# Kernel optimization log

Hardware: AMD Instinct MI355X
Metric: run time of the kernel (lower is better)

## Reference

```python
import jax, jax.numpy as jnp
import numpy as np

D_MODEL = 512
N_HEAD = 8
D_K = 64
D_V = 64
NUM_FEATURES = 266  # round(d_k * ln(d_k)) for d_k=64
KERNEL_EPS = 1e-4
NORM_STAB = 1e-6
LN_EPS = 1e-6


def _orthogonal_random_features():
    # blocks of transposed Q factors of Gaussian matrices, scaled by sqrt(d_k)
    rng = np.random.default_rng(0)
    blocks, rows = [], NUM_FEATURES
    while rows > 0:
        g = rng.standard_normal((D_K, D_K)).astype(np.float32)
        qm, _ = np.linalg.qr(g)
        blocks.append(qm.T[: min(rows, D_K)])
        rows -= D_K
    rf = np.concatenate(blocks, axis=0) * np.sqrt(D_K)
    return jnp.asarray(rf, dtype=jnp.float32)  # [m, d_k]


def _xavier(key, fan_in, fan_out):
    a = np.sqrt(6.0 / (fan_in + fan_out))
    return jax.random.uniform(key, (fan_in, fan_out), jnp.float32, -a, a)


def setup_inputs() -> dict:
    key = jax.random.key(0)
    ks = jax.random.split(key, 9)
    B, N = 1, 2048
    return {
        "q": jax.random.normal(ks[0], (B, N, D_MODEL), jnp.float32),
        "k": jax.random.normal(ks[1], (B, N, D_MODEL), jnp.float32),
        "v": jax.random.normal(ks[2], (B, N, D_MODEL), jnp.float32),
        "Wq": _xavier(ks[3], D_MODEL, N_HEAD * D_K),
        "Wk": _xavier(ks[4], D_MODEL, N_HEAD * D_K),
        "Wv": _xavier(ks[5], D_MODEL, N_HEAD * D_V),
        "W_fc": _xavier(ks[6], N_HEAD * D_V, D_MODEL),
        "b_fc": jnp.zeros((D_MODEL,), jnp.float32),
        "gamma": jnp.ones((D_MODEL,), jnp.float32),
        "beta": jnp.zeros((D_MODEL,), jnp.float32),
        "rf": _orthogonal_random_features(),
    }


def reference(q, k, v, Wq, Wk, Wv, W_fc, b_fc, gamma, beta, rf):
    B, N, _ = q.shape
    residual = q
    # pre-layernorm on queries only (normalize_before=True)
    mu = jnp.mean(q, axis=-1, keepdims=True)
    var = jnp.mean((q - mu) ** 2, axis=-1, keepdims=True)
    qn = (q - mu) * jax.lax.rsqrt(var + LN_EPS) * gamma + beta

    def heads(x, W, d):
        return (x @ W).reshape(B, N, N_HEAD, d).transpose(0, 2, 1, 3)

    qh = heads(qn, Wq, D_K)   # [b,h,n,dk]
    kh = heads(k, Wk, D_K)
    vh = heads(v, Wv, D_V)    # [b,h,n,dv]

    scale = D_MODEL ** (-0.25)
    qh = qh * scale
    kh = kh * scale

    proj_q = jnp.einsum('bhnd,md->bhnm', qh, rf)  # [b,h,n,m]
    proj_k = jnp.einsum('bhnd,md->bhnm', kh, rf)
    h_q = -0.5 * jnp.sum(qh ** 2, axis=-1, keepdims=True)  # [b,h,n,1]
    h_k = -0.5 * jnp.sum(kh ** 2, axis=-1, keepdims=True)

    # per-query stabilizer is h_q itself (last dim of h_q has size 1)
    q_kernel = jnp.exp(h_q + (proj_q - h_q))
    k_stab = jnp.max(h_k)  # global max stabilizer for keys
    k_kernel = jnp.exp(h_k + (proj_k - k_stab))

    c = NUM_FEATURES ** (-0.5)
    q_prime = c * (q_kernel + KERNEL_EPS)
    k_prime = c * (k_kernel + KERNEL_EPS)

    # causal linear attention via prefix sums
    D_inv = 1.0 / jnp.einsum('bhnm,bhnm->bhn', q_prime, jnp.cumsum(k_prime, axis=2))
    context = jnp.cumsum(jnp.einsum('bhnm,bhne->bhnme', k_prime, vh), axis=2)  # [b,h,n,m,dv]
    out = jnp.einsum('bhnme,bhnm,bhn->bhne', context, q_prime, D_inv)

    # output normalization with stabilizer
    d = jnp.einsum('bhnm,bhm->bhn', q_prime, jnp.sum(k_prime, axis=2))[..., None]
    d = d + 2.0 * NORM_STAB * (jnp.abs(d) <= NORM_STAB).astype(d.dtype)
    out = out / d

    out = out.transpose(0, 2, 1, 3).reshape(B, N, N_HEAD * D_V)
    return out @ W_fc + b_fc + residual
```

## Files before the change

kernel.cpp:

```cpp
#include <hip/hip_runtime.h>
#include <hip/hip_bf16.h>
#include <math.h>

#define DMODEL 512
#define NSEQ 2048
#define NHEAD 8
#define DK 64
#define DV 64
#define MFEAT 266
#define MPAD 288
#define NT 32
#define LN_EPS 1e-6f
#define KERNEL_EPS 1e-4f
#define NORM_STAB 1e-6f
#define SCALE 0.21022410381342863f

typedef __attribute__((ext_vector_type(8))) short short8;
typedef __attribute__((ext_vector_type(4))) short sv4;
typedef __attribute__((ext_vector_type(4))) float f32x4;

__device__ inline short f2bf(float f) {
    return (short)__bfloat16_as_ushort(__float2bfloat16(f));
}
__device__ inline float bf2f(short s) {
    unsigned u = ((unsigned)(unsigned short)s) << 16;
    return __builtin_bit_cast(float, u);
}

__global__ __launch_bounds__(256) void prep_kernel(const float* __restrict__ Wq,
                                                   const float* __restrict__ Wk,
                                                   const float* __restrict__ Wv,
                                                   const float* __restrict__ Wfc,
                                                   const float* __restrict__ rf,
                                                   short* __restrict__ Wqt,
                                                   short* __restrict__ Wkt,
                                                   short* __restrict__ Wvt,
                                                   short* __restrict__ Wfct,
                                                   short* __restrict__ rfb) {
    int wsel = blockIdx.z;
    int tid = threadIdx.x;
    if (wsel == 4) {
        if (blockIdx.x != 0) return;
        int r0 = blockIdx.y * 36;
        for (int lp = 0; lp < 9; ++lp) {
            int c = tid + lp * 256;
            int r = r0 + c / 64, d = c % 64;
            float v = (r < MFEAT) ? rf[(size_t)r * DK + d] : 0.f;
            rfb[(size_t)r * DK + d] = f2bf(v);
        }
        return;
    }
    __shared__ short T[64][65];
    int k0 = blockIdx.x * 64, n0 = blockIdx.y * 64;
    const float* W = (wsel == 0) ? Wq : (wsel == 1) ? Wk : (wsel == 2) ? Wv : Wfc;
    short* Wt = (wsel == 0) ? Wqt : (wsel == 1) ? Wkt : (wsel == 2) ? Wvt : Wfct;
    float scale = (wsel <= 1) ? SCALE : 1.f;
    for (int lp = 0; lp < 4; ++lp) {
        int c = tid + lp * 256;
        int kk = c >> 4, q4 = (c & 15) * 4;
        f32x4 v = *(const f32x4*)&W[(size_t)(k0 + kk) * DMODEL + n0 + q4];
        for (int j = 0; j < 4; ++j) T[q4 + j][kk] = f2bf(v[j] * scale);
    }
    __syncthreads();
    for (int lp = 0; lp < 2; ++lp) {
        int c = tid + lp * 256;
        int nn = c >> 3, c8 = c & 7;
        short8 v = *(const short8*)&T[nn][c8 * 8];
        *(short8*)&Wt[(size_t)(n0 + nn) * DMODEL + k0 + c8 * 8] = v;
    }
}

__global__ __launch_bounds__(256) void qkvfeat_kernel(const float* __restrict__ qx,
                                                      const float* __restrict__ kx,
                                                      const float* __restrict__ vx,
                                                      const short* __restrict__ Wqt,
                                                      const short* __restrict__ Wkt,
                                                      const short* __restrict__ Wvt,
                                                      const float* __restrict__ gamma,
                                                      const float* __restrict__ beta,
                                                      const short* __restrict__ rfb,
                                                      short* __restrict__ vh,
                                                      short* __restrict__ qp,
                                                      short* __restrict__ kp) {
    __shared__ __align__(16) char smem[38656];
    auto AsB = (short(*)[40])smem;
    auto BsB = (short(*)[40])(smem + 10240);
    auto Xs = (short(*)[72])smem;
    short* kpl = (short*)smem;
    float* hks = (float*)(smem + 38400);

    int z = blockIdx.z;
    const float* A = (z == 0) ? qx : (z == 1) ? kx : vx;
    const short* Bt = (z == 0) ? Wqt : (z == 1) ? Wkt : Wvt;
    int nt = blockIdx.x, h = blockIdx.y;
    int bm = nt * 64, bn = h * 64, n0 = nt * 64;
    int tid = threadIdx.x;
    int wid = tid >> 6, lane = tid & 63;
    f32x4 acc[4] = {f32x4{0,0,0,0}, f32x4{0,0,0,0}, f32x4{0,0,0,0}, f32x4{0,0,0,0}};
    int ar = tid >> 2, akq = tid & 3;
    float lnm = 0.f, lnr = 0.f;
    if (z == 0) {
        const float* xr = qx + (size_t)(bm + ar) * DMODEL + akq * 128;
        float s = 0.f, ss = 0.f;
#pragma unroll 4
        for (int i = 0; i < 128; i += 4) {
            f32x4 vv = *(const f32x4*)(xr + i);
            s += vv[0] + vv[1] + vv[2] + vv[3];
            ss += vv[0]*vv[0] + vv[1]*vv[1] + vv[2]*vv[2] + vv[3]*vv[3];
        }
        s += __shfl_xor(s, 1); s += __shfl_xor(s, 2);
        ss += __shfl_xor(ss, 1); ss += __shfl_xor(ss, 2);
        float m = s / (float)DMODEL;
        float var = ss / (float)DMODEL - m * m;
        lnm = m;
        lnr = rsqrtf(var + LN_EPS);
    }
    auto loadA = [&](int k0) -> short8 {
        const float* src = A + (size_t)(bm + ar) * DMODEL + k0 + akq * 8;
        f32x4 v0 = *(const f32x4*)src;
        f32x4 v1 = *(const f32x4*)(src + 4);
        short8 sv;
        if (z == 0) {
            f32x4 g0 = *(const f32x4*)&gamma[k0 + akq * 8];
            f32x4 g1 = *(const f32x4*)&gamma[k0 + akq * 8 + 4];
            f32x4 bb0 = *(const f32x4*)&beta[k0 + akq * 8];
            f32x4 bb1 = *(const f32x4*)&beta[k0 + akq * 8 + 4];
            for (int j = 0; j < 4; ++j) {
                sv[j] = f2bf((v0[j] - lnm) * lnr * g0[j] + bb0[j]);
                sv[4 + j] = f2bf((v1[j] - lnm) * lnr * g1[j] + bb1[j]);
            }
        } else {
            for (int j = 0; j < 4; ++j) { sv[j] = f2bf(v0[j]); sv[4 + j] = f2bf(v1[j]); }
        }
        return sv;
    };
    auto loadB = [&](int k0) -> short8 {
        return *(const short8*)&Bt[(size_t)(bn + ar) * DMODEL + k0 + akq * 8];
    };
    short8 aR0 = loadA(0), bR0 = loadB(0);
    short8 aR1 = loadA(32), bR1 = loadB(32);
    int buf = 0;
#pragma unroll 2
    for (int k0 = 0; k0 < DMODEL; k0 += 32) {
        int slot = (k0 >> 5) & 1;
        if (slot == 0) {
            *(short8*)&AsB[buf * 64 + ar][akq * 8] = aR0;
            *(short8*)&BsB[buf * 64 + ar][akq * 8] = bR0;
        } else {
            *(short8*)&AsB[buf * 64 + ar][akq * 8] = aR1;
            *(short8*)&BsB[buf * 64 + ar][akq * 8] = bR1;
        }
        __syncthreads();
        if (k0 + 64 < DMODEL) {
            if (slot == 0) { aR0 = loadA(k0 + 64); bR0 = loadB(k0 + 64); }
            else           { aR1 = loadA(k0 + 64); bR1 = loadB(k0 + 64); }
        }
        int row = buf * 64 + wid * 16 + (lane & 15);
        int koff = (lane >> 4) * 8;
        short8 a = *(const short8*)&AsB[row][koff];
        for (int nf = 0; nf < 4; ++nf) {
            int col = buf * 64 + nf * 16 + (lane & 15);
            short8 b = *(const short8*)&BsB[col][koff];
            acc[nf] = __builtin_amdgcn_mfma_f32_16x16x32_bf16(a, b, acc[nf], 0, 0, 0);
        }
        buf ^= 1;
    }
    __syncthreads();
    if (z == 2) {
        for (int nf = 0; nf < 4; ++nf) {
            int col = bn + nf * 16 + (lane & 15);
            for (int j = 0; j < 4; ++j) {
                int row = bm + wid * 16 + (lane >> 4) * 4 + j;
                vh[(size_t)row * DMODEL + col] = f2bf(acc[nf][j]);
            }
        }
        return;
    }
    for (int nf = 0; nf < 4; ++nf) {
        int col = nf * 16 + (lane & 15);
        for (int j = 0; j < 4; ++j) {
            int row = wid * 16 + (lane >> 4) * 4 + j;
            Xs[row][col] = f2bf(acc[nf][j]);
        }
    }
    if (z == 1) {
        for (int j = 0; j < 4; ++j) {
            float ss = 0.f;
            for (int nf = 0; nf < 4; ++nf) ss += acc[nf][j] * acc[nf][j];
            for (int o = 1; o < 16; o <<= 1) ss += __shfl_xor(ss, o);
            if ((lane & 15) == 0) hks[wid * 16 + (lane >> 4) * 4 + j] = -0.5f * ss;
        }
    }
    __syncthreads();

    int w = wid, l = lane;
    int fr = l & 15, fq = (l >> 4) * 8;
    short8 xb0 = *(const short8*)&Xs[w * 16 + fr][fq];
    short8 xb1 = *(const short8*)&Xs[w * 16 + fr][32 + fq];
    int n_loc = w * 16 + fr;
    float hval = (z == 1) ? hks[n_loc] : 0.f;
    __syncthreads();

    short (*kpl2)[300] = (short(*)[300])kpl;
    const float cnorm = 0.06131393394849658f;
#pragma unroll
    for (int tr = 0; tr < 18; ++tr) {
        int row = tr * 16 + fr;
        short8 a0 = *(const short8*)&rfb[(size_t)row * DK + fq];
        short8 a1 = *(const short8*)&rfb[(size_t)row * DK + 32 + fq];
        f32x4 facc = {0.f, 0.f, 0.f, 0.f};
        facc = __builtin_amdgcn_mfma_f32_16x16x32_bf16(a0, xb0, facc, 0, 0, 0);
        facc = __builtin_amdgcn_mfma_f32_16x16x32_bf16(a1, xb1, facc, 0, 0, 0);
        sv4 o;
        for (int j = 0; j < 4; ++j) {
            int m = tr * 16 + (l >> 4) * 4 + j;
            float val = (m < MFEAT) ? cnorm * (__expf(facc[j] + hval) + KERNEL_EPS) : 0.f;
            o[j] = f2bf(val);
        }
        *(sv4*)&kpl2[n_loc][tr * 16 + (l >> 4) * 4] = o;
    }
    __syncthreads();
    short* outp = (z == 0) ? qp : kp;
    for (int lp = 0; lp < 9; ++lp) {
        int c = tid + lp * 256;
        int nn = c / 36, c8 = c % 36;
        short8 v = *(const short8*)&kpl2[nn][c8 * 8];
        *(short8*)&outp[((size_t)h * NSEQ + n0 + nn) * MPAD + c8 * 8] = v;
    }
}

__global__ __launch_bounds__(256) void chunksum_kernel(const short* __restrict__ kp,
                                                       const short* __restrict__ vh,
                                                       short* __restrict__ KVc,
                                                       float* __restrict__ Ks) {
    int t = blockIdx.x, h = blockIdx.y;
    __shared__ short kpT[288 * 72];
    __shared__ short Vt[64][72];
    int tid = threadIdx.x;
    int w = tid >> 6, l = tid & 63;
    int fr = l & 15, fq8 = (l >> 4) * 8;
    const short* kpb = kp + ((size_t)h * NSEQ + (size_t)t * 64) * MPAD;

    for (int lp = 0; lp < 9; ++lp) {
        int c = tid + lp * 256;
        int i = c / 36, c8 = c % 36;
        short8 v = *(const short8*)&kpb[(size_t)i * MPAD + c8 * 8];
        int i8 = i >> 3, i7 = i & 7;
        for (int jj = 0; jj < 8; ++jj) {
            int m = c8 * 8 + jj;
            int ig = i8 ^ ((m >> 3) & 7);
            kpT[m * 72 + ig * 8 + i7] = v[jj];
        }
    }
    for (int lp = 0; lp < 2; ++lp) {
        int c = tid + lp * 256;
        int i = c & 63, d8 = (c >> 6) * 8;
        short8 v = *(const short8*)&vh[(size_t)(t * 64 + i) * DMODEL + h * DV + d8];
        for (int jj = 0; jj < 8; ++jj) Vt[d8 + jj][i] = v[jj];
    }
    __syncthreads();

    f32x4 acc[5][4];
#pragma unroll
    for (int tt = 0; tt < 5; ++tt)
        for (int nf = 0; nf < 4; ++nf) acc[tt][nf] = f32x4{0, 0, 0, 0};
#pragma unroll
    for (int tt = 0; tt < 5; ++tt) {
        int tr = w + tt * 4;
        if (tr < 18) {
            int row = tr * 16 + fr;
            int swz = (row >> 3) & 7;
            short8 a0 = *(const short8*)&kpT[row * 72 + (((fq8 >> 3)) ^ swz) * 8];
            short8 a1 = *(const short8*)&kpT[row * 72 + ((4 + (fq8 >> 3)) ^ swz) * 8];
            for (int nf = 0; nf < 4; ++nf) {
                short8 b0 = *(const short8*)&Vt[nf * 16 + fr][fq8];
                short8 b1 = *(const short8*)&Vt[nf * 16 + fr][32 + fq8];
                acc[tt][nf] = __builtin_amdgcn_mfma_f32_16x16x32_bf16(a0, b0, acc[tt][nf], 0, 0, 0);
                acc[tt][nf] = __builtin_amdgcn_mfma_f32_16x16x32_bf16(a1, b1, acc[tt][nf], 0, 0, 0);
            }
        }
    }
    for (int m = tid; m < MPAD; m += 256) {
        int swz = (m >> 3) & 7;
        float s = 0.f;
        for (int i8 = 0; i8 < 8; ++i8) {
            int ig = i8 ^ swz;
            for (int j = 0; j < 8; ++j) s += bf2f(kpT[m * 72 + ig * 8 + j]);
        }
        Ks[((size_t)h * NT + t) * MPAD + m] = s;
    }
    __syncthreads();
    short* kvT = kpT;
#pragma unroll
    for (int tt = 0; tt < 5; ++tt) {
        int tr = w + tt * 4;
        if (tr < 18) {
            for (int nf = 0; nf < 4; ++nf) {
                int dv = nf * 16 + fr;
                for (int j = 0; j < 4; ++j) {
                    int m = tr * 16 + (l >> 4) * 4 + j;
                    kvT[dv * 296 + m] = f2bf(acc[tt][nf][j]);
                }
            }
        }
    }
    __syncthreads();
    for (int lp = 0; lp < 9; ++lp) {
        int c = tid + lp * 256;
        int dv = c / 36, c8 = c % 36;
        short8 v = *(const short8*)&kvT[dv * 296 + c8 * 8];
        *(short8*)&KVc[(((size_t)h * NT + t) * DV + dv) * MPAD + c8 * 8] = v;
    }
}

__global__ __launch_bounds__(256) void scan_kernel(const short* __restrict__ KVc,
                                                   short* __restrict__ KVbT,
                                                   float* __restrict__ Ks,
                                                   float* __restrict__ Ktot) {
    int idx = blockIdx.x * 256 + threadIdx.x;
    const int NKV = NHEAD * DV * MPAD;
    if (idx < NKV) {
        int h = idx / (DV * MPAD);
        int rem = idx % (DV * MPAD);
        size_t base = (size_t)h * NT * DV * MPAD + rem;
        short vals[NT];
#pragma unroll
        for (int t = 0; t < NT; ++t) vals[t] = KVc[base + (size_t)t * DV * MPAD];
        float run = 0.f;
#pragma unroll
        for (int t = 0; t < NT; ++t) {
            KVbT[base + (size_t)t * DV * MPAD] = f2bf(run);
            run += bf2f(vals[t]);
        }
    } else {
        int j = idx - NKV;
        if (j < NHEAD * MPAD) {
            int h = j / MPAD, m = j % MPAD;
            size_t base = (size_t)h * NT * MPAD + m;
            float vals[NT];
#pragma unroll
            for (int t = 0; t < NT; ++t) vals[t] = Ks[base + (size_t)t * MPAD];
            float run = 0.f;
#pragma unroll
            for (int t = 0; t < NT; ++t) {
                Ks[base + (size_t)t * MPAD] = run;
                run += vals[t];
            }
            Ktot[(size_t)h * MPAD + m] = run;
        }
    }
}

__global__ __launch_bounds__(256) void phasec_kernel(const short* __restrict__ qp,
                                                     const short* __restrict__ kp,
                                                     const short* __restrict__ vh,
                                                     const short* __restrict__ KVbT,
                                                     const float* __restrict__ Ks,
                                                     const float* __restrict__ Ktot,
                                                     short* __restrict__ attn) {
    int t = blockIdx.x, h = blockIdx.y;
    __shared__ short Buf[64][296];
    __shared__ short Vt[64][72];
    __shared__ short Am[64][72];
    __shared__ float Ksp[MPAD], Ktp[MPAD];
    __shared__ float fscale_s[64];
    int tid = threadIdx.x;
    int w = tid >> 6, l = tid & 63;
    int fr = l & 15, fq = (l >> 4) * 8;
    const short* qpb = qp + ((size_t)h * NSEQ + (size_t)t * 64) * MPAD;
    const short* kpb = kp + ((size_t)h * NSEQ + (size_t)t * 64) * MPAD;
    const short* stb = KVbT + ((size_t)h * NT + t) * DV * MPAD;

    short8 qf[9];
#pragma unroll
    for (int ks = 0; ks < 9; ++ks)
        qf[ks] = *(const short8*)&qpb[(size_t)(w * 16 + fr) * MPAD + ks * 32 + fq];

    int srow = tid >> 2, sc4 = tid & 3;
#pragma unroll
    for (int lp = 0; lp < 9; ++lp) {
        int c = sc4 + lp * 4;
        *(short8*)&Buf[srow][c * 8] = *(const short8*)&kpb[(size_t)srow * MPAD + c * 8];
    }
    for (int lp = 0; lp < 2; ++lp) {
        int c = tid + lp * 256;
        int i = c & 63, d8 = (c >> 6) * 8;
        short8 v = *(const short8*)&vh[(size_t)(t * 64 + i) * DMODEL + h * DV + d8];
        for (int jj = 0; jj < 8; ++jj) Vt[d8 + jj][i] = v[jj];
    }
    for (int idx = tid; idx < MPAD; idx += 256) {
        Ksp[idx] = Ks[((size_t)h * NT + t) * MPAD + idx];
        Ktp[idx] = Ktot[(size_t)h * MPAD + idx];
    }
    short8 stg[9];
#pragma unroll
    for (int lp = 0; lp < 9; ++lp) {
        int c = sc4 + lp * 4;
        stg[lp] = *(const short8*)&stb[(size_t)srow * MPAD + c * 8];
    }
    __syncthreads();

    f32x4 accA[4] = {f32x4{0,0,0,0}, f32x4{0,0,0,0}, f32x4{0,0,0,0}, f32x4{0,0,0,0}};
    f32x4 accO[4] = {f32x4{0,0,0,0}, f32x4{0,0,0,0}, f32x4{0,0,0,0}, f32x4{0,0,0,0}};
#pragma unroll 3
    for (int ks = 0; ks < 9; ++ks) {
        int ko = ks * 32 + fq;
        for (int nf = 0; nf < 4; ++nf) {
            short8 bk = *(const short8*)&Buf[nf * 16 + fr][ko];
            accA[nf] = __builtin_amdgcn_mfma_f32_16x16x32_bf16(qf[ks], bk, accA[nf], 0, 0, 0);
        }
    }
    __syncthreads();
#pragma unroll
    for (int lp = 0; lp < 9; ++lp) {
        int c = sc4 + lp * 4;
        *(short8*)&Buf[srow][c * 8] = stg[lp];
    }
    for (int nf = 0; nf < 4; ++nf) {
        int col = nf * 16 + fr;
        for (int j = 0; j < 4; ++j) {
            int row = w * 16 + (l >> 4) * 4 + j;
            Am[row][col] = (col <= row) ? f2bf(accA[nf][j]) : (short)0;
        }
    }
    __syncthreads();
#pragma unroll 3
    for (int ks = 0; ks < 9; ++ks) {
        int ko = ks * 32 + fq;
        for (int nf = 0; nf < 4; ++nf) {
            short8 bs = *(const short8*)&Buf[nf * 16 + fr][ko];
            accO[nf] = __builtin_amdgcn_mfma_f32_16x16x32_bf16(qf[ks], bs, accO[nf], 0, 0, 0);
        }
    }
#pragma unroll
    for (int ks = 0; ks < 2; ++ks) {
        int ko = ks * 32 + fq;
        short8 a = *(const short8*)&Am[w * 16 + fr][ko];
        for (int nf = 0; nf < 4; ++nf) {
            short8 b = *(const short8*)&Vt[nf * 16 + fr][ko];
            accO[nf] = __builtin_amdgcn_mfma_f32_16x16x32_bf16(a, b, accO[nf], 0, 0, 0);
        }
    }
    int di = tid >> 2, dp = tid & 3;
    float dc = 0.f, df = 0.f;
    {
        const short* amrow = &Am[di][dp * 16];
        short8 s0 = *(const short8*)amrow;
        short8 s1 = *(const short8*)(amrow + 8);
        for (int j2 = 0; j2 < 8; ++j2) dc += bf2f(s0[j2]) + bf2f(s1[j2]);
    }
#pragma unroll
    for (int c8 = 0; c8 < 9; ++c8) {
        int m = dp * 72 + c8 * 8;
        short8 qv = *(const short8*)&qpb[(size_t)di * MPAD + m];
        for (int j2 = 0; j2 < 8; ++j2) {
            float qq = bf2f(qv[j2]);
            dc += qq * Ksp[m + j2];
            df += qq * Ktp[m + j2];
        }
    }
    dc += __shfl_xor(dc, 1); dc += __shfl_xor(dc, 2);
    df += __shfl_xor(df, 1); df += __shfl_xor(df, 2);
    if (dp == 0) {
        float dst = df;
        if (fabsf(dst) <= NORM_STAB) dst += 2.f * NORM_STAB;
        fscale_s[di] = (1.f / dc) / dst;
    }
    __syncthreads();
    for (int nf = 0; nf < 4; ++nf) {
        int col = nf * 16 + fr;
        for (int j = 0; j < 4; ++j) {
            int row = w * 16 + (l >> 4) * 4 + j;
            attn[((size_t)t * 64 + row) * DMODEL + h * DV + col] =
                f2bf(accO[nf][j] * fscale_s[row]);
        }
    }
}

__global__ __launch_bounds__(256) void fgemm_kernel(const short* __restrict__ A,
                                                    const short* __restrict__ Bt,
                                                    float* __restrict__ C,
                                                    const float* __restrict__ bias,
                                                    const float* __restrict__ residual) {
    __shared__ short AsB[128][40];
    __shared__ short BsB[128][40];
    int bm = blockIdx.y * 64, bn = blockIdx.x * 64;
    int tid = threadIdx.x;
    int wid = tid >> 6, lane = tid & 63;
    f32x4 acc[4] = {f32x4{0,0,0,0}, f32x4{0,0,0,0}, f32x4{0,0,0,0}, f32x4{0,0,0,0}};
    int ar = tid >> 2, akq = tid & 3;
    auto ldA = [&](int k0) { return *(const short8*)&A[(size_t)(bm + ar) * DMODEL + k0 + akq * 8]; };
    auto ldB = [&](int k0) { return *(const short8*)&Bt[(size_t)(bn + ar) * DMODEL + k0 + akq * 8]; };
    short8 aR0 = ldA(0), bR0 = ldB(0);
    short8 aR1 = ldA(32), bR1 = ldB(32);
    int buf = 0;
#pragma unroll 2
    for (int k0 = 0; k0 < DMODEL; k0 += 32) {
        int slot = (k0 >> 5) & 1;
        if (slot == 0) {
            *(short8*)&AsB[buf * 64 + ar][akq * 8] = aR0;
            *(short8*)&BsB[buf * 64 + ar][akq * 8] = bR0;
        } else {
            *(short8*)&AsB[buf * 64 + ar][akq * 8] = aR1;
            *(short8*)&BsB[buf * 64 + ar][akq * 8] = bR1;
        }
        __syncthreads();
        if (k0 + 64 < DMODEL) {
            if (slot == 0) { aR0 = ldA(k0 + 64); bR0 = ldB(k0 + 64); }
            else           { aR1 = ldA(k0 + 64); bR1 = ldB(k0 + 64); }
        }
        int row = buf * 64 + wid * 16 + (lane & 15);
        int koff = (lane >> 4) * 8;
        short8 a = *(const short8*)&AsB[row][koff];
        for (int nf = 0; nf < 4; ++nf) {
            int col = buf * 64 + nf * 16 + (lane & 15);
            short8 b = *(const short8*)&BsB[col][koff];
            acc[nf] = __builtin_amdgcn_mfma_f32_16x16x32_bf16(a, b, acc[nf], 0, 0, 0);
        }
        buf ^= 1;
    }
    for (int nf = 0; nf < 4; ++nf) {
        int col = bn + nf * 16 + (lane & 15);
        for (int j = 0; j < 4; ++j) {
            int row = bm + wid * 16 + (lane >> 4) * 4 + j;
            C[(size_t)row * DMODEL + col] =
                acc[nf][j] + bias[col] + residual[(size_t)row * DMODEL + col];
        }
    }
}

extern "C" void kernel_launch(void* const* d_in, const int* in_sizes, int n_in,
                              void* d_out, int out_size, void* d_ws, size_t ws_size,
                              hipStream_t stream) {
    const float* q = (const float*)d_in[0];
    const float* k = (const float*)d_in[1];
    const float* v = (const float*)d_in[2];
    const float* Wq = (const float*)d_in[3];
    const float* Wk = (const float*)d_in[4];
    const float* Wv = (const float*)d_in[5];
    const float* Wfc = (const float*)d_in[6];
    const float* bfc = (const float*)d_in[7];
    const float* gamma = (const float*)d_in[8];
    const float* beta = (const float*)d_in[9];
    const float* rf = (const float*)d_in[10];
    float* out = (float*)d_out;

    float* ws = (float*)d_ws;
    short* attn = (short*)ws;
    short* vhb = attn + (size_t)NSEQ * DMODEL;
    short* qp = vhb + (size_t)NSEQ * DMODEL;
    short* kp = qp + (size_t)NHEAD * NSEQ * MPAD;
    short* KVc = kp + (size_t)NHEAD * NSEQ * MPAD;
    short* KVbT = KVc + (size_t)NHEAD * NT * DV * MPAD;
    float* Ks = (float*)(KVbT + (size_t)NHEAD * NT * DV * MPAD);
    float* Ktot = Ks + (size_t)NHEAD * NT * MPAD;
    short* Wqt = (short*)(Ktot + (size_t)NHEAD * MPAD);
    short* Wkt = Wqt + (size_t)DMODEL * DMODEL;
    short* Wvt = Wkt + (size_t)DMODEL * DMODEL;
    short* Wfct = Wvt + (size_t)DMODEL * DMODEL;
    short* rfb = Wfct + (size_t)DMODEL * DMODEL;

    dim3 gp(8, 8, 5);
    prep_kernel<<<gp, 256, 0, stream>>>(Wq, Wk, Wv, Wfc, rf, Wqt, Wkt, Wvt, Wfct, rfb);
    dim3 gq(NT, NHEAD, 3);
    qkvfeat_kernel<<<gq, 256, 0, stream>>>(q, k, v, Wqt, Wkt, Wvt, gamma, beta, rfb,
                                           vhb, qp, kp);
    dim3 ga(NT, NHEAD);
    chunksum_kernel<<<ga, 256, 0, stream>>>(kp, vhb, KVc, Ks);
    int scan_threads = NHEAD * DV * MPAD + NHEAD * MPAD;
    scan_kernel<<<(scan_threads + 255) / 256, 256, 0, stream>>>(KVc, KVbT, Ks, Ktot);
    dim3 gc(NT, NHEAD);
    phasec_kernel<<<gc, 256, 0, stream>>>(qp, kp, vhb, KVbT, Ks, Ktot, attn);
    dim3 g(DMODEL / 64, NSEQ / 64);
    fgemm_kernel<<<g, 256, 0, stream>>>(attn, Wfct, out, bfc, q);
}
```

Baseline: 70.49 us.

## Halve qkvfeat row tile to 32 rows and split waves over columns and features

The fused QKV projection and feature kernel now handles 32 sequence rows per block instead of 64, which doubles the grid to 64x8x3 blocks. The four waves are rearranged into a 2x2 grid over rows and output columns, and the feature loop is split between wave pairs. The squared norm for the key stabiliser is reduced across waves through shared memory. The aim is more blocks, better occupancy and less shared memory per block on a small problem. The cost is more redundant weight and rf loads per output row and a shallower register prefetch (one stage instead of two).

```diff
diff --git a/kernel.cpp b/kernel.cpp
--- a/kernel.cpp
+++ b/kernel.cpp
@@ -82,130 +82,116 @@
                                                       short* __restrict__ vh,
                                                       short* __restrict__ qp,
                                                       short* __restrict__ kp) {
-    __shared__ __align__(16) char smem[38656];
+    __shared__ __align__(16) char smem[19712];
     auto AsB = (short(*)[40])smem;
-    auto BsB = (short(*)[40])(smem + 10240);
+    auto BsB = (short(*)[40])(smem + 5120);
     auto Xs = (short(*)[72])smem;
     short* kpl = (short*)smem;
-    float* hks = (float*)(smem + 38400);
+    float* hks = (float*)(smem + 19200);
+    float* hpart = (float*)(smem + 19328);
 
     int z = blockIdx.z;
     const float* A = (z == 0) ? qx : (z == 1) ? kx : vx;
     const short* Bt = (z == 0) ? Wqt : (z == 1) ? Wkt : Wvt;
     int nt = blockIdx.x, h = blockIdx.y;
-    int bm = nt * 64, bn = h * 64, n0 = nt * 64;
+    int bm = nt * 32, bn = h * 64;
     int tid = threadIdx.x;
     int wid = tid >> 6, lane = tid & 63;
-    f32x4 acc[4] = {f32x4{0,0,0,0}, f32x4{0,0,0,0}, f32x4{0,0,0,0}, f32x4{0,0,0,0}};
-    int ar = tid >> 2, akq = tid & 3;
+    int fr = lane & 15, fq = (lane >> 4) * 8;
+    int rt = wid & 1, cfb = (wid >> 1) * 2;
+    f32x4 acc[2] = {f32x4{0,0,0,0}, f32x4{0,0,0,0}};
+    int arow = tid >> 3, ak = tid & 7;
+    int nrow = tid >> 2, bk = (tid & 3) * 8;
     float lnm = 0.f, lnr = 0.f;
     if (z == 0) {
-        const float* xr = qx + (size_t)(bm + ar) * DMODEL + akq * 128;
+        const float* xr = qx + (size_t)(bm + arow) * DMODEL + ak * 64;
         float s = 0.f, ss = 0.f;
 #pragma unroll 4
-        for (int i = 0; i < 128; i += 4) {
+        for (int i = 0; i < 64; i += 4) {
             f32x4 vv = *(const f32x4*)(xr + i);
             s += vv[0] + vv[1] + vv[2] + vv[3];
             ss += vv[0]*vv[0] + vv[1]*vv[1] + vv[2]*vv[2] + vv[3]*vv[3];
         }
-        s += __shfl_xor(s, 1); s += __shfl_xor(s, 2);
-        ss += __shfl_xor(ss, 1); ss += __shfl_xor(ss, 2);
+        s += __shfl_xor(s, 1); s += __shfl_xor(s, 2); s += __shfl_xor(s, 4);
+        ss += __shfl_xor(ss, 1); ss += __shfl_xor(ss, 2); ss += __shfl_xor(ss, 4);
         float m = s / (float)DMODEL;
         float var = ss / (float)DMODEL - m * m;
         lnm = m;
         lnr = rsqrtf(var + LN_EPS);
     }
-    auto loadA = [&](int k0) -> short8 {
-        const float* src = A + (size_t)(bm + ar) * DMODEL + k0 + akq * 8;
-        f32x4 v0 = *(const f32x4*)src;
-        f32x4 v1 = *(const f32x4*)(src + 4);
-        short8 sv;
+    auto loadA = [&](int k0) -> sv4 {
+        f32x4 v0 = *(const f32x4*)&A[(size_t)(bm + arow) * DMODEL + k0 + ak * 4];
+        sv4 sv;
         if (z == 0) {
-            f32x4 g0 = *(const f32x4*)&gamma[k0 + akq * 8];
-            f32x4 g1 = *(const f32x4*)&gamma[k0 + akq * 8 + 4];
-            f32x4 bb0 = *(const f32x4*)&beta[k0 + akq * 8];
-            f32x4 bb1 = *(const f32x4*)&beta[k0 + akq * 8 + 4];
-            for (int j = 0; j < 4; ++j) {
-                sv[j] = f2bf((v0[j] - lnm) * lnr * g0[j] + bb0[j]);
-                sv[4 + j] = f2bf((v1[j] - lnm) * lnr * g1[j] + bb1[j]);
-            }
+            f32x4 g0 = *(const f32x4*)&gamma[k0 + ak * 4];
+            f32x4 b0 = *(const f32x4*)&beta[k0 + ak * 4];
+            for (int j = 0; j < 4; ++j)
+                sv[j] = f2bf((v0[j] - lnm) * lnr * g0[j] + b0[j]);
         } else {
-            for (int j = 0; j < 4; ++j) { sv[j] = f2bf(v0[j]); sv[4 + j] = f2bf(v1[j]); }
+            for (int j = 0; j < 4; ++j) sv[j] = f2bf(v0[j]);
         }
         return sv;
     };
     auto loadB = [&](int k0) -> short8 {
-        return *(const short8*)&Bt[(size_t)(bn + ar) * DMODEL + k0 + akq * 8];
+        return *(const short8*)&Bt[(size_t)(bn + nrow) * DMODEL + k0 + bk];
     };
-    short8 aR0 = loadA(0), bR0 = loadB(0);
-    short8 aR1 = loadA(32), bR1 = loadB(32);
+    sv4 aReg = loadA(0);
+    short8 bReg = loadB(0);
     int buf = 0;
 #pragma unroll 2
     for (int k0 = 0; k0 < DMODEL; k0 += 32) {
-        int slot = (k0 >> 5) & 1;
-        if (slot == 0) {
-            *(short8*)&AsB[buf * 64 + ar][akq * 8] = aR0;
-            *(short8*)&BsB[buf * 64 + ar][akq * 8] = bR0;
-        } else {
-            *(short8*)&AsB[buf * 64 + ar][akq * 8] = aR1;
-            *(short8*)&BsB[buf * 64 + ar][akq * 8] = bR1;
-        }
+        *(sv4*)&AsB[buf * 32 + arow][ak * 4] = aReg;
+        *(short8*)&BsB[buf * 64 + nrow][bk] = bReg;
         __syncthreads();
-        if (k0 + 64 < DMODEL) {
-            if (slot == 0) { aR0 = loadA(k0 + 64); bR0 = loadB(k0 + 64); }
-            else           { aR1 = loadA(k0 + 64); bR1 = loadB(k0 + 64); }
-        }
-        int row = buf * 64 + wid * 16 + (lane & 15);
-        int koff = (lane >> 4) * 8;
-        short8 a = *(const short8*)&AsB[row][koff];
-        for (int nf = 0; nf < 4; ++nf) {
-            int col = buf * 64 + nf * 16 + (lane & 15);
-            short8 b = *(const short8*)&BsB[col][koff];
+        if (k0 + 32 < DMODEL) { aReg = loadA(k0 + 32); bReg = loadB(k0 + 32); }
+        short8 a = *(const short8*)&AsB[buf * 32 + rt * 16 + fr][fq];
+        for (int nf = 0; nf < 2; ++nf) {
+            short8 b = *(const short8*)&BsB[buf * 64 + (cfb + nf) * 16 + fr][fq];
             acc[nf] = __builtin_amdgcn_mfma_f32_16x16x32_bf16(a, b, acc[nf], 0, 0, 0);
         }
         buf ^= 1;
     }
     __syncthreads();
     if (z == 2) {
-        for (int nf = 0; nf < 4; ++nf) {
-            int col = bn + nf * 16 + (lane & 15);
+        for (int nf = 0; nf < 2; ++nf) {
+            int col = bn + (cfb + nf) * 16 + fr;
             for (int j = 0; j < 4; ++j) {
-                int row = bm + wid * 16 + (lane >> 4) * 4 + j;
+                int row = bm + rt * 16 + (lane >> 4) * 4 + j;
                 vh[(size_t)row * DMODEL + col] = f2bf(acc[nf][j]);
             }
         }
         return;
     }
-    for (int nf = 0; nf < 4; ++nf) {
-        int col = nf * 16 + (lane & 15);
-        for (int j = 0; j < 4; ++j) {
-            int row = wid * 16 + (lane >> 4) * 4 + j;
-            Xs[row][col] = f2bf(acc[nf][j]);
-        }
+    for (int nf = 0; nf < 2; ++nf) {
+        int col = (cfb + nf) * 16 + fr;
+        for (int j = 0; j < 4; ++j)
+            Xs[rt * 16 + (lane >> 4) * 4 + j][col] = f2bf(acc[nf][j]);
     }
     if (z == 1) {
         for (int j = 0; j < 4; ++j) {
-            float ss = 0.f;
-            for (int nf = 0; nf < 4; ++nf) ss += acc[nf][j] * acc[nf][j];
+            float ss = acc[0][j] * acc[0][j] + acc[1][j] * acc[1][j];
             for (int o = 1; o < 16; o <<= 1) ss += __shfl_xor(ss, o);
-            if ((lane & 15) == 0) hks[wid * 16 + (lane >> 4) * 4 + j] = -0.5f * ss;
-        }
-    }
-    __syncthreads();
-
-    int w = wid, l = lane;
-    int fr = l & 15, fq = (l >> 4) * 8;
-    short8 xb0 = *(const short8*)&Xs[w * 16 + fr][fq];
-    short8 xb1 = *(const short8*)&Xs[w * 16 + fr][32 + fq];
-    int n_loc = w * 16 + fr;
+            if (fr == 0) hpart[(rt * 16 + (lane >> 4) * 4 + j) * 2 + (wid >> 1)] = ss;
+        }
+    }
+    __syncthreads();
+    if (z == 1 && tid < 32)
+        hks[tid] = -0.5f * (hpart[tid * 2] + hpart[tid * 2 + 1]);
+    __syncthreads();
+
+    int nb = wid & 1, mpar = wid >> 1;
+    int n_loc = nb * 16 + fr;
+    short8 xb0 = *(const short8*)&Xs[n_loc][fq];
+    short8 xb1 = *(const short8*)&Xs[n_loc][32 + fq];
     float hval = (z == 1) ? hks[n_loc] : 0.f;
     __syncthreads();
 
     short (*kpl2)[300] = (short(*)[300])kpl;
     const float cnorm = 0.06131393394849658f;
 #pragma unroll
-    for (int tr = 0; tr < 18; ++tr) {
-        int row = tr * 16 + fr;
+    for (int t = 0; t < 9; ++t) {
+        int mt = mpar + 2 * t;
+        int row = mt * 16 + fr;
         short8 a0 = *(const short8*)&rfb[(size_t)row * DK + fq];
         short8 a1 = *(const short8*)&rfb[(size_t)row * DK + 32 + fq];
         f32x4 facc = {0.f, 0.f, 0.f, 0.f};
@@ -213,19 +199,21 @@
         facc = __builtin_amdgcn_mfma_f32_16x16x32_bf16(a1, xb1, facc, 0, 0, 0);
         sv4 o;
         for (int j = 0; j < 4; ++j) {
-            int m = tr * 16 + (l >> 4) * 4 + j;
+            int m = mt * 16 + (lane >> 4) * 4 + j;
             float val = (m < MFEAT) ? cnorm * (__expf(facc[j] + hval) + KERNEL_EPS) : 0.f;
             o[j] = f2bf(val);
         }
-        *(sv4*)&kpl2[n_loc][tr * 16 + (l >> 4) * 4] = o;
+        *(sv4*)&kpl2[n_loc][mt * 16 + (lane >> 4) * 4] = o;
     }
     __syncthreads();
     short* outp = (z == 0) ? qp : kp;
-    for (int lp = 0; lp < 9; ++lp) {
-        int c = tid + lp * 256;
-        int nn = c / 36, c8 = c % 36;
-        short8 v = *(const short8*)&kpl2[nn][c8 * 8];
-        *(short8*)&outp[((size_t)h * NSEQ + n0 + nn) * MPAD + c8 * 8] = v;
+    for (int lp = 0; lp < 5; ++lp) {
+        int c = tid + lp * 256;
+        if (c < 1152) {
+            int nn = c / 36, c8 = c % 36;
+            short8 v = *(const short8*)&kpl2[nn][c8 * 8];
+            *(short8*)&outp[((size_t)h * NSEQ + bm + nn) * MPAD + c8 * 8] = v;
+        }
     }
 }
 
@@ -562,7 +550,7 @@
 
     dim3 gp(8, 8, 5);
     prep_kernel<<<gp, 256, 0, stream>>>(Wq, Wk, Wv, Wfc, rf, Wqt, Wkt, Wvt, Wfct, rfb);
-    dim3 gq(NT, NHEAD, 3);
+    dim3 gq(NSEQ / 32, NHEAD, 3);
     qkvfeat_kernel<<<gq, 256, 0, stream>>>(q, k, v, Wqt, Wkt, Wvt, gamma, beta, rfb,
                                            vhb, qp, kp);
     dim3 ga(NT, NHEAD);
```

Result: no change. 70.56 us (+0.1%).
